# Kernel tuning notes

Measured on AMD Instinct MI355X. Metric: run time of the kernel, lower is better.

The kernel has to match this reference:

```python
import jax, jax.numpy as jnp
import numpy as np

N_DIM = 32  # latent_dim + action_dim

# Static index sets matching the original Python loop order (i<=j, i<=j<=k)
_PI, _PJ = np.triu_indices(N_DIM)  # row-major i then j, matches loop order
_TRIPLES = np.array([(a, b, c) for a in range(N_DIM)
                     for b in range(a, N_DIM)
                     for c in range(b, N_DIM)], dtype=np.int32)
_TI, _TJ, _TK = _TRIPLES[:, 0], _TRIPLES[:, 1], _TRIPLES[:, 2]


def setup_inputs() -> dict:
    key = jax.random.key(0)
    z = jax.random.normal(key, (8192, N_DIM), dtype=jnp.float32)
    return {"z": z}


def reference(z):
    B = z.shape[0]
    ones = jnp.ones((B, 1), dtype=z.dtype)
    pairs = z[:, _PI] * z[:, _PJ]                      # (B, 528)
    triples = z[:, _TI] * z[:, _TJ] * z[:, _TK]        # (B, 5984)
    library = jnp.concatenate([ones, z, pairs, triples, jnp.sin(z)], axis=1)
    return library  # (B, 6577)
```

## Files before the change

### kernel.cpp

```cpp
#include <hip/hip_runtime.h>
#include <math.h>

#define NDIM   32
#define NPAIRS 528
#define NTRIP  5984
#define NCOLS  (1 + NDIM + NPAIRS + NTRIP + NDIM)
#define ONE_IDX 64

struct Tbl { unsigned int v[NCOLS]; };

constexpr Tbl make_tbl() {
    Tbl t{};
    int c = 0;
    const unsigned ONE = ONE_IDX;
    t.v[c++] = ONE | (ONE << 7) | (ONE << 14);
    for (unsigned i = 0; i < NDIM; ++i)
        t.v[c++] = i | (ONE << 7) | (ONE << 14);
    for (unsigned i = 0; i < NDIM; ++i)
        for (unsigned j = i; j < NDIM; ++j)
            t.v[c++] = i | (j << 7) | (ONE << 14);
    for (unsigned a = 0; a < NDIM; ++a)
        for (unsigned b = a; b < NDIM; ++b)
            for (unsigned k = b; k < NDIM; ++k)
                t.v[c++] = a | (b << 7) | (k << 14);
    for (unsigned i = 0; i < NDIM; ++i)
        t.v[c++] = (NDIM + i) | (ONE << 7) | (ONE << 14);
    return t;
}

__device__ __constant__ Tbl TBL = make_tbl();

__global__ __launch_bounds__(256)
void sindy_library_kernel(const float* __restrict__ z, float* __restrict__ out) {
    __shared__ float w[ONE_IDX + 1];
    const int row = blockIdx.x;
    const int tid = threadIdx.x;

    if (tid < NDIM) {
        float v = z[row * NDIM + tid];
        w[tid]        = v;
        w[NDIM + tid] = sinf(v);
    }
    if (tid == 255) w[ONE_IDX] = 1.0f;
    __syncthreads();

    const long long base = (long long)row * NCOLS;
    for (int c = tid; c < NCOLS; c += 256) {
        const unsigned e = TBL.v[c];
        const float v = w[e & 127] * w[(e >> 7) & 127] * w[(e >> 14) & 127];
        __builtin_nontemporal_store(v, &out[base + c]);
    }
}

extern "C" void kernel_launch(void* const* d_in, const int* in_sizes, int n_in,
                              void* d_out, int out_size, void* d_ws, size_t ws_size,
                              hipStream_t stream) {
    const float* z = (const float*)d_in[0];
    float* out     = (float*)d_out;
    const int rows = in_sizes[0] / NDIM;
    sindy_library_kernel<<<rows, 256, 0, stream>>>(z, out);
}
```

Baseline: 253.3 us.

## Flatten output into grid-stride float4 stores with per-element z fetch

Replaces the one-block-per-row kernel, which staged z and sin(z) in shared memory, with a flat grid-stride kernel. Each thread computes four consecutive output elements, handling row boundaries, and writes them as one float4 store. Factors are read straight from global z, and sin is recomputed per use instead of once per row. It drops the shared memory and barrier in exchange for more redundant global reads and sinf calls. It also drops the nontemporal store hint and leaves any remainder when the total is not a multiple of 4 unwritten.

```diff
diff --git a/kernel.cpp b/kernel.cpp
--- a/kernel.cpp
+++ b/kernel.cpp
@@ -30,25 +30,32 @@
 
 __device__ __constant__ Tbl TBL = make_tbl();
 
+__device__ __forceinline__ float fetch(const float* __restrict__ zr, unsigned i) {
+    if (i < 32u)  return zr[i];
+    if (i < 64u)  return sinf(zr[i - 32u]);
+    return 1.0f;
+}
+
 __global__ __launch_bounds__(256)
-void sindy_library_kernel(const float* __restrict__ z, float* __restrict__ out) {
-    __shared__ float w[ONE_IDX + 1];
-    const int row = blockIdx.x;
-    const int tid = threadIdx.x;
+void sindy_flat_kernel(const float* __restrict__ z, float* __restrict__ out,
+                       int total4) {
+    const int stride = gridDim.x * 256;
+    for (int idx = blockIdx.x * 256 + threadIdx.x; idx < total4; idx += stride) {
+        const unsigned f = (unsigned)idx * 4u;
+        unsigned row = f / NCOLS;
+        unsigned col = f - row * NCOLS;
+        const float* zr = z + row * NDIM;
 
-    if (tid < NDIM) {
-        float v = z[row * NDIM + tid];
-        w[tid]        = v;
-        w[NDIM + tid] = sinf(v);
-    }
-    if (tid == 255) w[ONE_IDX] = 1.0f;
-    __syncthreads();
-
-    const long long base = (long long)row * NCOLS;
-    for (int c = tid; c < NCOLS; c += 256) {
-        const unsigned e = TBL.v[c];
-        const float v = w[e & 127] * w[(e >> 7) & 127] * w[(e >> 14) & 127];
-        __builtin_nontemporal_store(v, &out[base + c]);
+        float v[4];
+#pragma unroll
+        for (int j = 0; j < 4; ++j) {
+            const unsigned e = TBL.v[col];
+            v[j] = fetch(zr, e & 127u) * fetch(zr, (e >> 7) & 127u)
+                 * fetch(zr, (e >> 14) & 127u);
+            ++col;
+            if (col == NCOLS) { col = 0; zr += NDIM; }
+        }
+        *reinterpret_cast<float4*>(out + f) = make_float4(v[0], v[1], v[2], v[3]);
     }
 }
 
@@ -57,6 +64,9 @@
                               hipStream_t stream) {
     const float* z = (const float*)d_in[0];
     float* out     = (float*)d_out;
-    const int rows = in_sizes[0] / NDIM;
-    sindy_library_kernel<<<rows, 256, 0, stream>>>(z, out);
+    const int rows   = in_sizes[0] / NDIM;
+    const int total  = rows * NCOLS;
+    const int total4 = total / 4;
+    const int blocks = 2048;
+    sindy_flat_kernel<<<blocks, 256, 0, stream>>>(z, out, total4);
 }
```

After: 269.0 us. 6.2% more time.
